# Kernel optimization log

Hardware: AMD Instinct MI355X
Metric: run time of the kernel (lower is better)

Reference implementation:

```python
import jax, jax.numpy as jnp
import numpy as np

N_NODES = 100000
N_EDGES = 1600000
DIM_IN, DIM_HID, DIM_OUT = 64, 128, 40


def setup_inputs() -> dict:
    key = jax.random.key(0)
    ks = jax.random.split(key, 6)
    x = jax.random.normal(ks[0], (N_NODES, DIM_IN), dtype=jnp.float32)
    edge_index = jax.random.randint(ks[1], (2, N_EDGES), 0, N_NODES, dtype=jnp.int64)
    s_in = 1.0 / np.sqrt(DIM_IN)
    s_hid = 1.0 / np.sqrt(DIM_HID)
    W1l = jax.random.normal(ks[2], (DIM_HID, DIM_IN), dtype=jnp.float32) * s_in
    W1r = jax.random.normal(ks[3], (DIM_HID, DIM_IN), dtype=jnp.float32) * s_in
    b1 = jnp.zeros((DIM_HID,), dtype=jnp.float32)
    W2l = jax.random.normal(ks[4], (DIM_OUT, DIM_HID), dtype=jnp.float32) * s_hid
    W2r = jax.random.normal(ks[5], (DIM_OUT, DIM_HID), dtype=jnp.float32) * s_hid
    b2 = jnp.zeros((DIM_OUT,), dtype=jnp.float32)
    return {"x": x, "edge_index": edge_index, "W1l": W1l, "b1": b1,
            "W1r": W1r, "W2l": W2l, "b2": b2, "W2r": W2r}


def _sage_conv(h, src, dst, Wl, bl, Wr, n_nodes):
    # mean aggregation of source-node features into target nodes
    msg = h[src]                                      # [E, d]
    agg = jax.ops.segment_sum(msg, dst, num_segments=n_nodes)
    cnt = jax.ops.segment_sum(jnp.ones((src.shape[0],), h.dtype), dst,
                              num_segments=n_nodes)
    agg = agg / jnp.maximum(cnt, 1.0)[:, None]        # [N, d]
    # PyG SAGEConv: lin_l(agg) + bias + lin_r(x) (root weight, no bias)
    return agg @ Wl.T + bl + h @ Wr.T


def reference(x, edge_index, W1l, b1, W1r, W2l, b2, W2r):
    src, dst = edge_index[0], edge_index[1]
    n = x.shape[0]
    h = _sage_conv(x, src, dst, W1l, b1, W1r, n)
    h = jax.nn.relu(h)
    out = _sage_conv(h, src, dst, W2l, b2, W2r, n)
    return jax.nn.log_softmax(out, axis=-1)
```

## Files before the change

### kernel.cpp

```cpp
#include <hip/hip_runtime.h>
#include <math.h>

#define NN 100000
#define DI 64
#define DH 128
#define DO 40

#define NPB_C 256
#define NBUCK_C 391
#define CAP_C 4608
#define COLCAP 1856
#define EPB 4096
#define TPB_S 512
#define KE (EPB / TPB_S)

typedef __attribute__((ext_vector_type(8))) short bf16x8;
typedef __attribute__((ext_vector_type(4))) float f32x4;
typedef __attribute__((ext_vector_type(2))) float f32x2;

__device__ __forceinline__ unsigned short bf16r(float a) {
    unsigned u = __float_as_uint(a);
    u = (u + 0x7FFF + ((u >> 16) & 1)) >> 16;
    return (unsigned short)u;
}
__device__ __forceinline__ unsigned bf16pair(float a, float b) {
    return (unsigned)bf16r(a) | ((unsigned)bf16r(b) << 16);
}
__device__ __forceinline__ float bflo(unsigned u) { return __uint_as_float(u << 16); }
__device__ __forceinline__ float bfhi(unsigned u) { return __uint_as_float(u & 0xFFFF0000u); }

__global__ __launch_bounds__(TPB_S) void setup_scatter_kernel(
        const float* __restrict__ x, const float* __restrict__ W1l,
        const float* __restrict__ W1r, const float* __restrict__ W2l,
        const float* __restrict__ W2r,
        unsigned* __restrict__ xb, unsigned short* __restrict__ xgs,
        unsigned short* __restrict__ WB1,
        unsigned short* __restrict__ WB2, unsigned* __restrict__ p2,
        const int* __restrict__ src, const int* __restrict__ dst,
        int* __restrict__ bcur, int* __restrict__ eb,
        int nbe, int E, int N) {
    __shared__ int h[NBUCK_C];
    int t = threadIdx.x;
    if ((int)blockIdx.x < nbe) {
        if (t < NBUCK_C) h[t] = 0;
        __syncthreads();
        int base = blockIdx.x * EPB;
        int end = base + EPB; if (end > E) end = E;
        int dloc[KE];
#pragma unroll
        for (int k = 0; k < KE; k++) {
            int i = base + t + k * TPB_S;
            dloc[k] = (i < end) ? dst[i] : -1;
        }
#pragma unroll
        for (int k = 0; k < KE; k++)
            if (dloc[k] >= 0) atomicAdd(&h[(unsigned)dloc[k] >> 8], 1);
        __syncthreads();
        if (t < NBUCK_C) {
            int v = h[t];
            h[t] = v ? (atomicAdd(&bcur[t], v) + t * CAP_C) : 0;
        }
        __syncthreads();
#pragma unroll
        for (int k = 0; k < KE; k++) {
            int d = dloc[k];
            if (d >= 0) {
                unsigned bk = (unsigned)d >> 8;
                int local = d & 255;
                int pos = atomicAdd(&h[bk], 1);
                eb[pos] = (local << 17) | src[base + t + k * TPB_S];
            }
        }
    } else {
        int idx = (blockIdx.x - nbe) * TPB_S + t;
        if (idx < (N + 1) * 32) {
            if (idx < N * 32) {
                float2 f = ((const float2*)x)[idx];
                xb[idx] = bf16pair(f.x, f.y);
                xgs[idx] = (unsigned short)
                    __builtin_amdgcn_cvt_pk_fp8_f32(f.x, f.y, 0u, false);
            } else {
                xb[idx] = 0;
                xgs[idx] = 0;
            }
        }
        if (idx < 16384) {
            int j = idx & 7, lane = (idx >> 3) & 63, ks = (idx >> 9) & 3, nt = idx >> 11;
            int k = ks * 32 + (lane >> 4) * 8 + j;
            int n = nt * 16 + (lane & 15);
            float v = (k < DI) ? W1l[n * DI + k] : W1r[n * DI + (k - DI)];
            WB1[idx] = bf16r(v);
        }
        if (idx >= 16384 && idx < 16384 + 10240) {
            int idx2 = idx - 16384;
            int j = idx2 & 7, lane = (idx2 >> 3) & 63, ks = (idx2 >> 9) & 3, nt = idx2 >> 11;
            int k = ks * 32 + (lane >> 4) * 8 + j;
            int n = nt * 16 + (lane & 15);
            float v = (n < DO) ? W2l[n * DH + k] : W2r[(n - DO) * DH + k];
            WB2[idx2] = bf16r(v);
        }
        if (idx < 10) p2[(size_t)N * 10 + idx] = 0;
    }
}

__global__ __launch_bounds__(256) void agg_gemm12_kernel(
        const unsigned* __restrict__ xb, const unsigned short* __restrict__ xgs,
        const int* __restrict__ eb, const int* __restrict__ bend,
        int* __restrict__ rowptr, int* __restrict__ cntg, float* __restrict__ invg,
        int* __restrict__ colg,
        const unsigned short* __restrict__ WB1, const float* __restrict__ b1,
        const unsigned short* __restrict__ WB2, const float* __restrict__ b2,
        unsigned* __restrict__ p2, unsigned short* __restrict__ selfpb, int N) {
    __shared__ unsigned short sh[64][136];
    __shared__ __align__(16) int col_l[COLCAP];
    __shared__ int scnt[64], sbase[64], scur[64];
    __shared__ int stot;
    int t = threadIdx.x;
    int b = blockIdx.x;
    int cb = b >> 2, sub = b & 3;
    int cnt_b = bend[cb];
    size_t ebeg = (size_t)cb * CAP_C;

    if (t < 64) scnt[t] = 0;
    __syncthreads();
    for (int i = t; i < cnt_b; i += 256) {
        int loc = eb[ebeg + i] >> 17;
        if ((loc >> 6) == sub) atomicAdd(&scnt[loc & 63], 1);
    }
    __syncthreads();
    if (t < 64) {
        int c = scnt[t];
        int pc = (c + 7) & ~7;
        int scan = pc;
#pragma unroll
        for (int off = 1; off < 64; off <<= 1) {
            int u = __shfl_up(scan, off);
            if (t >= off) scan += u;
        }
        int base = scan - pc;
        sbase[t] = base;
        scur[t] = base;
        if (t == 63) stot = scan;
        int node = b * 64 + t;
        if (node < N) {
            rowptr[node] = b * COLCAP + base;
            cntg[node] = c;
            invg[node] = 1.0f / (float)(c > 0 ? c : 1);
        }
    }
    __syncthreads();
    for (int i = t; i < cnt_b; i += 256) {
        int pk = eb[ebeg + i];
        int loc = pk >> 17;
        if ((loc >> 6) == sub) {
            int pos = atomicAdd(&scur[loc & 63], 1);
            col_l[pos] = pk & 0x1FFFF;
        }
    }
    __syncthreads();
    if (t < 64) {
        int c = scnt[t], pc = (c + 7) & ~7, base = sbase[t];
        for (int i = c; i < pc; i++) col_l[base + i] = NN;
    }
    __syncthreads();
    {
        int tot = stot;
        for (int i = t; i < tot; i += 256)
            colg[(size_t)b * COLCAP + i] = col_l[i];
    }

    int w = t >> 6, lane = t & 63;
    int lw = w * 16;
    int g8 = (t >> 3) & 7;
    int chunk = t & 7;
    int rbase = b * 64 + lw;
#pragma unroll
    for (int it = 0; it < 2; ++it) {
        int lr = lw + g8 + it * 8;
        int n = b * 64 + lr;
        bool valid = (n < N);
        int ne = valid ? n : NN;
        float a[8];
#pragma unroll
        for (int j = 0; j < 8; j++) a[j] = 0.f;
        float invn = 0.f;
        if (valid) {
            int beg = sbase[lr], deg = scnt[lr];
            int degp = (deg + 3) & ~3;
            for (int i = 0; i < degp; i += 4) {
                int4 c4 = *(const int4*)(col_l + beg + i);
                uint2 g0 = *(const uint2*)(xgs + (size_t)c4.x * 32 + chunk * 4);
                uint2 g1 = *(const uint2*)(xgs + (size_t)c4.y * 32 + chunk * 4);
                uint2 g2 = *(const uint2*)(xgs + (size_t)c4.z * 32 + chunk * 4);
                uint2 g3 = *(const uint2*)(xgs + (size_t)c4.w * 32 + chunk * 4);
                f32x2 d;
                d = __builtin_amdgcn_cvt_pk_f32_fp8(g0.x, false); a[0] += d.x; a[1] += d.y;
                d = __builtin_amdgcn_cvt_pk_f32_fp8(g0.x, true);  a[2] += d.x; a[3] += d.y;
                d = __builtin_amdgcn_cvt_pk_f32_fp8(g0.y, false); a[4] += d.x; a[5] += d.y;
                d = __builtin_amdgcn_cvt_pk_f32_fp8(g0.y, true);  a[6] += d.x; a[7] += d.y;
                d = __builtin_amdgcn_cvt_pk_f32_fp8(g1.x, false); a[0] += d.x; a[1] += d.y;
                d = __builtin_amdgcn_cvt_pk_f32_fp8(g1.x, true);  a[2] += d.x; a[3] += d.y;
                d = __builtin_amdgcn_cvt_pk_f32_fp8(g1.y, false); a[4] += d.x; a[5] += d.y;
                d = __builtin_amdgcn_cvt_pk_f32_fp8(g1.y, true);  a[6] += d.x; a[7] += d.y;
                d = __builtin_amdgcn_cvt_pk_f32_fp8(g2.x, false); a[0] += d.x; a[1] += d.y;
                d = __builtin_amdgcn_cvt_pk_f32_fp8(g2.x, true);  a[2] += d.x; a[3] += d.y;
                d = __builtin_amdgcn_cvt_pk_f32_fp8(g2.y, false); a[4] += d.x; a[5] += d.y;
                d = __builtin_amdgcn_cvt_pk_f32_fp8(g2.y, true);  a[6] += d.x; a[7] += d.y;
                d = __builtin_amdgcn_cvt_pk_f32_fp8(g3.x, false); a[0] += d.x; a[1] += d.y;
                d = __builtin_amdgcn_cvt_pk_f32_fp8(g3.x, true);  a[2] += d.x; a[3] += d.y;
                d = __builtin_amdgcn_cvt_pk_f32_fp8(g3.y, false); a[4] += d.x; a[5] += d.y;
                d = __builtin_amdgcn_cvt_pk_f32_fp8(g3.y, true);  a[6] += d.x; a[7] += d.y;
            }
            invn = 1.0f / (float)(deg > 0 ? deg : 1);
        }
        uint4 u = *(const uint4*)(xb + (size_t)ne * 32 + chunk * 4);
        uint4 o;
        o.x = bf16pair(a[0] * invn, a[1] * invn);
        o.y = bf16pair(a[2] * invn, a[3] * invn);
        o.z = bf16pair(a[4] * invn, a[5] * invn);
        o.w = bf16pair(a[6] * invn, a[7] * invn);
        *(uint4*)&sh[lr][chunk * 8] = o;
        *(uint4*)&sh[lr][64 + chunk * 8] = u;
    }
    asm volatile("" ::: "memory");

    int quad = lane >> 4, m = lane & 15;
    f32x4 acc[8];
#pragma unroll
    for (int nt = 0; nt < 8; nt++) acc[nt] = (f32x4)(0.f);
#pragma unroll
    for (int ks = 0; ks < 4; ks++) {
        bf16x8 a = *(const bf16x8*)(&sh[lw + m][ks * 32 + quad * 8]);
#pragma unroll
        for (int nt = 0; nt < 8; nt++) {
            bf16x8 bb = *(const bf16x8*)(WB1 + ((size_t)(nt * 4 + ks) * 64 + lane) * 8);
            acc[nt] = __builtin_amdgcn_mfma_f32_16x16x32_bf16(a, bb, acc[nt], 0, 0, 0);
        }
    }
    asm volatile("" ::: "memory");
#pragma unroll
    for (int nt = 0; nt < 8; nt++) {
        int colj = nt * 16 + m;
        float bj = b1[colj];
#pragma unroll
        for (int r = 0; r < 4; r++) {
            sh[lw + quad * 4 + r][colj] = bf16r(fmaxf(acc[nt][r] + bj, 0.f));
        }
    }
    asm volatile("" ::: "memory");

    f32x4 acc2[5];
#pragma unroll
    for (int nt = 0; nt < 5; nt++) acc2[nt] = (f32x4)(0.f);
#pragma unroll
    for (int ks = 0; ks < 4; ks++) {
        bf16x8 a = *(const bf16x8*)(&sh[lw + m][ks * 32 + quad * 8]);
#pragma unroll
        for (int nt = 0; nt < 5; nt++) {
            bf16x8 bb = *(const bf16x8*)(WB2 + ((size_t)(nt * 4 + ks) * 64 + lane) * 8);
            acc2[nt] = __builtin_amdgcn_mfma_f32_16x16x32_bf16(a, bb, acc2[nt], 0, 0, 0);
        }
    }
    asm volatile("" ::: "memory");
    float* stw = (float*)&sh[lw][0];
#pragma unroll
    for (int nt = 0; nt < 5; nt++) {
        int colj = nt * 16 + m;
#pragma unroll
        for (int r = 0; r < 4; r++) {
            int row = rbase + quad * 4 + r;
            float v = acc2[nt][r];
            if (colj < 40) {
                stw[(quad * 4 + r) * 41 + colj] = v;
            } else if (row < N) {
                selfpb[(size_t)row * 40 + (colj - 40)] = bf16r(v + b2[colj - 40]);
            }
        }
    }
    asm volatile("" ::: "memory");
    for (int i = lane; i < 160; i += 64) {
        int lr = i / 10, dw = i - lr * 10;
        int grow = rbase + lr;
        if (grow < N) {
            float v0 = stw[lr * 41 + dw * 4 + 0], v1 = stw[lr * 41 + dw * 4 + 1];
            float v2 = stw[lr * 41 + dw * 4 + 2], v3 = stw[lr * 41 + dw * 4 + 3];
            unsigned u = __builtin_amdgcn_cvt_pk_fp8_f32(v0, v1, 0u, false);
            u = __builtin_amdgcn_cvt_pk_fp8_f32(v2, v3, u, true);
            p2[(size_t)grow * 10 + dw] = u;
        }
    }
}

__global__ void agg2_softmax_kernel(const unsigned* __restrict__ p2,
                                    const unsigned short* __restrict__ selfpb,
                                    const int* __restrict__ rowptr,
                                    const int* __restrict__ cnt,
                                    const float* __restrict__ inv,
                                    const int* __restrict__ col,
                                    float* __restrict__ out, int N) {
    int n = (blockIdx.x * 256 + threadIdx.x) >> 3;
    int chunk = threadIdx.x & 7;
    if (n >= N) return;
    int beg = rowptr[n], deg = cnt[n];
    int degp = (deg + 7) & ~7;
    bool vc = (chunk < 5);
    float a[8];
#pragma unroll
    for (int j = 0; j < 8; j++) a[j] = 0.f;
    for (int i = 0; i < degp; i += 8) {
        int ss[8];
#pragma unroll
        for (int k = 0; k < 8; k++) ss[k] = col[beg + i + k];
        if (vc) {
            uint2 uu[8];
#pragma unroll
            for (int k = 0; k < 8; k++)
                uu[k] = *(const uint2*)(p2 + (size_t)ss[k] * 10 + chunk * 2);
#pragma unroll
            for (int k = 0; k < 8; k++) {
                f32x2 d;
                d = __builtin_amdgcn_cvt_pk_f32_fp8(uu[k].x, false); a[0] += d.x; a[1] += d.y;
                d = __builtin_amdgcn_cvt_pk_f32_fp8(uu[k].x, true);  a[2] += d.x; a[3] += d.y;
                d = __builtin_amdgcn_cvt_pk_f32_fp8(uu[k].y, false); a[4] += d.x; a[5] += d.y;
                d = __builtin_amdgcn_cvt_pk_f32_fp8(uu[k].y, true);  a[6] += d.x; a[7] += d.y;
            }
        }
    }
    float invn = inv[n];
    float v[8];
    if (vc) {
        uint4 sv = *(const uint4*)(selfpb + (size_t)n * 40 + chunk * 8);
        v[0] = a[0] * invn + bflo(sv.x); v[1] = a[1] * invn + bfhi(sv.x);
        v[2] = a[2] * invn + bflo(sv.y); v[3] = a[3] * invn + bfhi(sv.y);
        v[4] = a[4] * invn + bflo(sv.z); v[5] = a[5] * invn + bfhi(sv.z);
        v[6] = a[6] * invn + bflo(sv.w); v[7] = a[7] * invn + bfhi(sv.w);
    } else {
#pragma unroll
        for (int j = 0; j < 8; j++) v[j] = 0.f;
    }
    float mv = -INFINITY;
    if (vc) {
#pragma unroll
        for (int j = 0; j < 8; j++) mv = fmaxf(mv, v[j]);
    }
#pragma unroll
    for (int off = 1; off <= 4; off <<= 1) mv = fmaxf(mv, __shfl_xor(mv, off, 8));
    float es = 0.f;
    if (vc) {
#pragma unroll
        for (int j = 0; j < 8; j++) es += expf(v[j] - mv);
    }
#pragma unroll
    for (int off = 1; off <= 4; off <<= 1) es += __shfl_xor(es, off, 8);
    if (vc) {
        float ls = mv + logf(es);
        float4 o0, o1;
        o0.x = v[0] - ls; o0.y = v[1] - ls; o0.z = v[2] - ls; o0.w = v[3] - ls;
        o1.x = v[4] - ls; o1.y = v[5] - ls; o1.z = v[6] - ls; o1.w = v[7] - ls;
        *(float4*)(out + (size_t)n * DO + chunk * 8) = o0;
        *(float4*)(out + (size_t)n * DO + chunk * 8 + 4) = o1;
    }
}

extern "C" void kernel_launch(void* const* d_in, const int* in_sizes, int n_in,
                              void* d_out, int out_size, void* d_ws, size_t ws_size,
                              hipStream_t stream) {
    const float* x   = (const float*)d_in[0];
    const int*  ei   = (const int*)d_in[1];
    const float* W1l = (const float*)d_in[2];
    const float* b1  = (const float*)d_in[3];
    const float* W1r = (const float*)d_in[4];
    const float* W2l = (const float*)d_in[5];
    const float* b2  = (const float*)d_in[6];
    const float* W2r = (const float*)d_in[7];
    float* out = (float*)d_out;

    const int E = in_sizes[1] / 2;
    const int N = NN;
    const int* src = ei;
    const int* dst = ei + E;
    const int nbe = (E + EPB - 1) / EPB;
    const int nsetup = ((N + 1) * 32 + TPB_S - 1) / TPB_S;
    const int nagg = (N + 63) / 64;

    size_t off = 0;
    auto alloc = [&](size_t nf) { size_t o = off; off += (nf + 63) & ~(size_t)63; return o; };
    size_t o_bcur   = alloc(NBUCK_C);
    size_t o_eb     = alloc((size_t)NBUCK_C * CAP_C);
    size_t o_colg   = alloc((size_t)nagg * COLCAP + 64);
    size_t o_rowptr = alloc(N);
    size_t o_cnt    = alloc(N);
    size_t o_inv    = alloc(N);
    size_t o_xb     = alloc((size_t)(N + 1) * 32);
    size_t o_xg     = alloc((size_t)(N + 1) * 16);
    size_t o_p2     = alloc((size_t)(N + 1) * 10);
    size_t o_selfp  = alloc((size_t)N * 20);
    size_t o_wb1    = alloc(16384 / 2);
    size_t o_wb2    = alloc(10240 / 2);
    (void)ws_size;

    float* ws = (float*)d_ws;
    int* bcur   = (int*)(ws + o_bcur);
    int* eb     = (int*)(ws + o_eb);
    int* colg   = (int*)(ws + o_colg);
    int* rowptr = (int*)(ws + o_rowptr);
    int* cnt    = (int*)(ws + o_cnt);
    float* inv  = ws + o_inv;
    unsigned* xb = (unsigned*)(ws + o_xb);
    unsigned short* xgs = (unsigned short*)(ws + o_xg);
    unsigned* p2 = (unsigned*)(ws + o_p2);
    unsigned short* selfpb = (unsigned short*)(ws + o_selfp);
    unsigned short* WB1 = (unsigned short*)(ws + o_wb1);
    unsigned short* WB2 = (unsigned short*)(ws + o_wb2);

    hipMemsetAsync(bcur, 0, NBUCK_C * sizeof(int), stream);

    setup_scatter_kernel<<<nbe + nsetup, TPB_S, 0, stream>>>(
        x, W1l, W1r, W2l, W2r, xb, xgs, WB1, WB2, p2, src, dst, bcur, eb, nbe, E, N);

    agg_gemm12_kernel<<<nagg, 256, 0, stream>>>(
        xb, xgs, eb, bcur, rowptr, cnt, inv, colg,
        WB1, b1, WB2, b2, p2, selfpb, N);

    agg2_softmax_kernel<<<(N * 8 + 255) / 256, 256, 0, stream>>>(
        p2, selfpb, rowptr, cnt, inv, colg, out, N);
}
```

Baseline: 193.8 us.

## Halve destination bucket size and cache bucket edges in registers

Destination buckets now cover 128 nodes instead of 256, so each 64-node aggregation block scans half as many packed edges from its bucket. The bucket's edge entries are loaded once into registers and reused for both the counting and the placement passes, instead of being read from global memory twice. In exchange there are twice as many buckets, more global cursor atomics, and a tighter per-bucket capacity that could overflow on skewed degree distributions.

```diff
diff --git a/kernel.cpp b/kernel.cpp
--- a/kernel.cpp
+++ b/kernel.cpp
@@ -6,13 +6,14 @@
 #define DH 128
 #define DO 40
 
-#define NPB_C 256
-#define NBUCK_C 391
-#define CAP_C 4608
+#define NPB_C 128
+#define NBUCK_C 782
+#define CAP_C 2560
 #define COLCAP 1856
 #define EPB 4096
 #define TPB_S 512
 #define KE (EPB / TPB_S)
+#define KE2 10
 
 typedef __attribute__((ext_vector_type(8))) short bf16x8;
 typedef __attribute__((ext_vector_type(4))) float f32x4;
@@ -42,7 +43,7 @@
     __shared__ int h[NBUCK_C];
     int t = threadIdx.x;
     if ((int)blockIdx.x < nbe) {
-        if (t < NBUCK_C) h[t] = 0;
+        for (int i = t; i < NBUCK_C; i += TPB_S) h[i] = 0;
         __syncthreads();
         int base = blockIdx.x * EPB;
         int end = base + EPB; if (end > E) end = E;
@@ -54,19 +55,19 @@
         }
 #pragma unroll
         for (int k = 0; k < KE; k++)
-            if (dloc[k] >= 0) atomicAdd(&h[(unsigned)dloc[k] >> 8], 1);
+            if (dloc[k] >= 0) atomicAdd(&h[(unsigned)dloc[k] >> 7], 1);
         __syncthreads();
-        if (t < NBUCK_C) {
-            int v = h[t];
-            h[t] = v ? (atomicAdd(&bcur[t], v) + t * CAP_C) : 0;
+        for (int i = t; i < NBUCK_C; i += TPB_S) {
+            int v = h[i];
+            h[i] = v ? (atomicAdd(&bcur[i], v) + i * CAP_C) : 0;
         }
         __syncthreads();
 #pragma unroll
         for (int k = 0; k < KE; k++) {
             int d = dloc[k];
             if (d >= 0) {
-                unsigned bk = (unsigned)d >> 8;
-                int local = d & 255;
+                unsigned bk = (unsigned)d >> 7;
+                int local = d & 127;
                 int pos = atomicAdd(&h[bk], 1);
                 eb[pos] = (local << 17) | src[base + t + k * TPB_S];
             }
@@ -117,15 +118,25 @@
     __shared__ int stot;
     int t = threadIdx.x;
     int b = blockIdx.x;
-    int cb = b >> 2, sub = b & 3;
+    int cb = b >> 1, sub = b & 1;
     int cnt_b = bend[cb];
     size_t ebeg = (size_t)cb * CAP_C;
 
+    int ec[KE2];
+#pragma unroll
+    for (int j = 0; j < KE2; j++) {
+        int i = t + j * 256;
+        ec[j] = (i < cnt_b) ? eb[ebeg + i] : -1;
+    }
     if (t < 64) scnt[t] = 0;
     __syncthreads();
-    for (int i = t; i < cnt_b; i += 256) {
-        int loc = eb[ebeg + i] >> 17;
-        if ((loc >> 6) == sub) atomicAdd(&scnt[loc & 63], 1);
+#pragma unroll
+    for (int j = 0; j < KE2; j++) {
+        int pk = ec[j];
+        if (pk >= 0) {
+            int loc = pk >> 17;
+            if ((loc >> 6) == sub) atomicAdd(&scnt[loc & 63], 1);
+        }
     }
     __syncthreads();
     if (t < 64) {
@@ -149,12 +160,15 @@
         }
     }
     __syncthreads();
-    for (int i = t; i < cnt_b; i += 256) {
-        int pk = eb[ebeg + i];
-        int loc = pk >> 17;
-        if ((loc >> 6) == sub) {
-            int pos = atomicAdd(&scur[loc & 63], 1);
-            col_l[pos] = pk & 0x1FFFF;
+#pragma unroll
+    for (int j = 0; j < KE2; j++) {
+        int pk = ec[j];
+        if (pk >= 0) {
+            int loc = pk >> 17;
+            if ((loc >> 6) == sub) {
+                int pos = atomicAdd(&scur[loc & 63], 1);
+                col_l[pos] = pk & 0x1FFFF;
+            }
         }
     }
     __syncthreads();
```

After: 186.9 us. 3.5% less time.
